# Optimization experiments

Measured on AMD Instinct MI355X. Metric: run time of the kernel, lower is better.

## Reference

```python
import jax, jax.numpy as jnp
import numpy as np

N_HEADS = 16
HEAD_DIM = 64
HIDDEN = N_HEADS * HEAD_DIM


def setup_inputs() -> dict:
    key = jax.random.key(0)
    ks = jax.random.split(key, 10)
    B, F, T = 2, 2048, 2048
    std = 0.02
    inp = {
        "from_tensor": jax.random.normal(ks[0], (B, F, HIDDEN), dtype=jnp.float32),
        "to_tensor": jax.random.normal(ks[1], (B, T, HIDDEN), dtype=jnp.float32),
        "attention_mask": jax.random.randint(ks[2], (B, F, T), 0, 2, dtype=jnp.int32),
        "Wq": jax.random.normal(ks[3], (HIDDEN, HIDDEN), dtype=jnp.float32) * std,
        "bq": jnp.zeros((HIDDEN,), dtype=jnp.float32),
        "Wk": jax.random.normal(ks[4], (HIDDEN, HIDDEN), dtype=jnp.float32) * std,
        "bk": jnp.zeros((HIDDEN,), dtype=jnp.float32),
        "Wv": jax.random.normal(ks[5], (HIDDEN, HIDDEN), dtype=jnp.float32) * std,
        "bv": jnp.zeros((HIDDEN,), dtype=jnp.float32),
    }
    return inp


def reference(from_tensor, to_tensor, attention_mask, Wq, bq, Wk, bk, Wv, bv):
    B, F, _ = from_tensor.shape
    T = to_tensor.shape[1]
    N, H = N_HEADS, HEAD_DIM

    # QKV projections (no activations: query/key/value act fns are None)
    q = (from_tensor @ Wq + bq).reshape(B, F, N, H)
    k = (to_tensor @ Wk + bk).reshape(B, T, N, H)
    v = (to_tensor @ Wv + bv).reshape(B, T, N, H)

    scores = jnp.einsum('BFNH,BTNH->BNFT', q, k) * (1.0 / np.sqrt(float(H)))
    # additive mask: mask [B,F,T] -> [B,1,F,T]; 0 entries get -10000
    adder = (1.0 - attention_mask.astype(jnp.float32))[:, None, :, :] * -10000.0
    scores = scores + adder
    probs = jax.nn.softmax(scores, axis=-1)  # dropout skipped (inference)

    context = jnp.einsum('BNFT,BTNH->BFNH', probs, v)
    return context.reshape(B, F, N * H)
```

## Files before the change

### kernel.cpp

```cpp
#include <hip/hip_runtime.h>


typedef short v8s __attribute__((ext_vector_type(8)));
typedef float v4f __attribute__((ext_vector_type(4)));
typedef unsigned short u16;
typedef unsigned int   u32;
typedef unsigned long long u64;

constexpr float QSCALE = 0.18033688011112042f;

__device__ __forceinline__ u16 f2bf(float f) {
    u32 u = __builtin_bit_cast(u32, f);
    u += 0x7fffu + ((u >> 16) & 1u);
    return (u16)(u >> 16);
}

__device__ __forceinline__ u32 pack_trunc(float a, float b) {
    return __builtin_amdgcn_perm(__builtin_bit_cast(u32, b),
                                 __builtin_bit_cast(u32, a), 0x07060302u);
}

__device__ __forceinline__ u32 pack_rnd(u32 ua, u32 ub) {
    ua += 0x7fffu + ((ua >> 16) & 1u);
    ub += 0x7fffu + ((ub >> 16) & 1u);
    return __builtin_amdgcn_perm(ub, ua, 0x07060302u);
}

__device__ __forceinline__ uint4 cvt8(uint4 lo, uint4 hi) {
    uint4 r;
    r.x = pack_rnd(lo.x, lo.y);
    r.y = pack_rnd(lo.z, lo.w);
    r.z = pack_rnd(hi.x, hi.y);
    r.w = pack_rnd(hi.z, hi.w);
    return r;
}

__device__ __forceinline__ v8s ld8(const u16* p) {
    return *reinterpret_cast<const v8s*>(p);
}

__global__ __launch_bounds__(256) void prep(
    const float* __restrict__ Wq, const float* __restrict__ Wk, const float* __restrict__ Wv,
    u16* __restrict__ Wqt, u16* __restrict__ Wkt, u16* __restrict__ Wvt,
    const int* __restrict__ mask, u64* __restrict__ words) {
    __shared__ float tile[32][33];
    const int bid = blockIdx.x, tid = threadIdx.x;
    if (bid < 3072) {
        const int zz = bid >> 10, rem = bid & 1023;
        const float* W = zz == 0 ? Wq : (zz == 1 ? Wk : Wv);
        u16* Wt = zz == 0 ? Wqt : (zz == 1 ? Wkt : Wvt);
        const int tx = tid & 31, ty = tid >> 5;
        const int n0 = (rem & 31) * 32, k0 = (rem >> 5) * 32;
        for (int i = 0; i < 4; i++)
            tile[ty + i * 8][tx] = W[(size_t)(k0 + ty + i * 8) * 1024 + n0 + tx];
        __syncthreads();
        for (int i = 0; i < 4; i++)
            Wt[(size_t)(n0 + ty + i * 8) * 1024 + k0 + tx] = f2bf(tile[tx][ty + i * 8]);
    } else {
        const int lane = tid & 63;
        const int g0 = (bid - 3072) * 32 + (tid >> 6) * 8;
        const int* mp = mask + (size_t)g0 * 64 + lane;
        u64* wp = words + g0;
        #pragma unroll
        for (int i = 0; i < 8; i++) {
            const u64 bits = __ballot(mp[(size_t)i * 64] != 0);
            if (lane == 0) wp[i] = bits;
        }
    }
}

__global__ __launch_bounds__(256, 3) void gemm_qkv(
    const float* __restrict__ Xf32, const float* __restrict__ Xt32,
    const u16* __restrict__ Wqt, const u16* __restrict__ Wkt, const u16* __restrict__ Wvt,
    const float* __restrict__ bq, const float* __restrict__ bk, const float* __restrict__ bv,
    u16* __restrict__ Qb, u16* __restrict__ Kb, u16* __restrict__ Vtb) {
    const int z = blockIdx.z;
    const float* A    = z == 0 ? Xf32 : Xt32;
    const u16* Bt     = z == 0 ? Wqt : (z == 1 ? Wkt : Wvt);
    const float* bias = z == 0 ? bq : (z == 1 ? bk : bv);
    u16* C            = z == 0 ? Qb : (z == 1 ? Kb : Vtb);
    const int mode    = (z == 2);
    const float sc    = (z == 0) ? QSCALE : 1.0f;

    __shared__ u16 As[2][128][32];
    __shared__ u16 Bs[2][128][32];
    const uint4* Ag = reinterpret_cast<const uint4*>(A);
    const uint4* Bg = reinterpret_cast<const uint4*>(Bt);

    const int tid = threadIdx.x;
    const int lane = tid & 63, wave = tid >> 6;
    const int quad = lane >> 4, l16 = lane & 15;
    const int wm = wave >> 1, wn = wave & 1;
    const int m0 = blockIdx.x * 128, n0 = blockIdx.y * 128;

    const int cg  = (lane & 3) ^ ((lane >> 3) & 3);
    const int sw8 = (quad ^ ((l16 >> 1) & 3)) * 8;

    const int gi0 = wave * 4;
    const uint4 *ap0, *ap1, *ap2, *ap3, *bp0, *bp1, *bp2, *bp3;
    {
        const int rl = lane >> 2;
        const int rb0 = ((gi0 + 0) & 7) * 16 + rl, kh0 = (gi0 + 0) >> 3;
        const int rb1 = ((gi0 + 1) & 7) * 16 + rl, kh1 = (gi0 + 1) >> 3;
        const int rb2 = ((gi0 + 2) & 7) * 16 + rl, kh2 = (gi0 + 2) >> 3;
        const int rb3 = ((gi0 + 3) & 7) * 16 + rl, kh3 = (gi0 + 3) >> 3;
        ap0 = Ag + (size_t)(m0 + rb0) * 256 + (kh0 * 4 + cg) * 2;
        ap1 = Ag + (size_t)(m0 + rb1) * 256 + (kh1 * 4 + cg) * 2;
        ap2 = Ag + (size_t)(m0 + rb2) * 256 + (kh2 * 4 + cg) * 2;
        ap3 = Ag + (size_t)(m0 + rb3) * 256 + (kh3 * 4 + cg) * 2;
        bp0 = Bg + (size_t)(n0 + rb0) * 128 + kh0 * 4 + cg;
        bp1 = Bg + (size_t)(n0 + rb1) * 128 + kh1 * 4 + cg;
        bp2 = Bg + (size_t)(n0 + rb2) * 128 + kh2 * 4 + cg;
        bp3 = Bg + (size_t)(n0 + rb3) * 128 + kh3 * 4 + cg;
    }
    uint4* da = reinterpret_cast<uint4*>((u16*)As + gi0 * 512) + lane;
    uint4* db = reinterpret_cast<uint4*>((u16*)Bs + gi0 * 512) + lane;

    v4f acc[4][4];
    for (int i = 0; i < 4; i++)
        for (int j = 0; j < 4; j++) acc[i][j] = (v4f)0.0f;

    uint4 a0l = ap0[0], a0h = ap0[1]; ap0 += 16;
    uint4 a1l = ap1[0], a1h = ap1[1]; ap1 += 16;
    uint4 a2l = ap2[0], a2h = ap2[1]; ap2 += 16;
    uint4 a3l = ap3[0], a3h = ap3[1]; ap3 += 16;
    uint4 sb0 = *bp0; bp0 += 8;
    uint4 sb1 = *bp1; bp1 += 8;
    uint4 sb2 = *bp2; bp2 += 8;
    uint4 sb3 = *bp3; bp3 += 8;
    uint4 ca0 = cvt8(a0l, a0h);
    uint4 ca1 = cvt8(a1l, a1h);
    uint4 ca2 = cvt8(a2l, a2h);
    uint4 ca3 = cvt8(a3l, a3h);

    for (int k0 = 0; k0 < 16; k0++) {
        __syncthreads();
        da[0]   = ca0;  da[64]  = ca1;  da[128] = ca2;  da[192] = ca3;
        db[0]   = sb0;  db[64]  = sb1;  db[128] = sb2;  db[192] = sb3;
        __syncthreads();

        if (k0 < 15) {
            a0l = ap0[0]; a0h = ap0[1]; ap0 += 16;
            a1l = ap1[0]; a1h = ap1[1]; ap1 += 16;
            a2l = ap2[0]; a2h = ap2[1]; ap2 += 16;
            a3l = ap3[0]; a3h = ap3[1]; ap3 += 16;
            sb0 = *bp0; bp0 += 8;
            sb1 = *bp1; bp1 += 8;
            sb2 = *bp2; bp2 += 8;
            sb3 = *bp3; bp3 += 8;
        }

        #pragma unroll
        for (int kk = 0; kk < 2; kk++) {
            v8s af[4], bf[4];
            #pragma unroll
            for (int mt = 0; mt < 4; mt++) af[mt] = ld8(&As[kk][wm * 64 + mt * 16 + l16][sw8]);
            #pragma unroll
            for (int nt = 0; nt < 4; nt++) bf[nt] = ld8(&Bs[kk][wn * 64 + nt * 16 + l16][sw8]);
            #pragma unroll
            for (int mt = 0; mt < 4; mt++)
                #pragma unroll
                for (int nt = 0; nt < 4; nt++)
                    acc[mt][nt] = __builtin_amdgcn_mfma_f32_16x16x32_bf16(af[mt], bf[nt], acc[mt][nt], 0, 0, 0);
        }

        if (k0 < 15) {
            ca0 = cvt8(a0l, a0h);
            ca1 = cvt8(a1l, a1h);
            ca2 = cvt8(a2l, a2h);
            ca3 = cvt8(a3l, a3h);
        }
    }

    #pragma unroll
    for (int nt = 0; nt < 4; nt++) {
        const int col = n0 + wn * 64 + nt * 16 + l16;
        const float bvv = bias[col];
        #pragma unroll
        for (int mt = 0; mt < 4; mt++) {
            const int mbase = m0 + wm * 64 + mt * 16 + quad * 4;
            if (mode == 0) {
                for (int r = 0; r < 4; r++)
                    C[(size_t)(mbase + r) * 1024 + col] = f2bf((acc[mt][nt][r] + bvv) * sc);
            } else {
                const int b = mbase >> 11, t = mbase & 2047;
                const int head = col >> 6, h = col & 63;
                ushort4 pk;
                pk.x = f2bf(acc[mt][nt][0] + bvv);
                pk.y = f2bf(acc[mt][nt][1] + bvv);
                pk.z = f2bf(acc[mt][nt][2] + bvv);
                pk.w = f2bf(acc[mt][nt][3] + bvv);
                *reinterpret_cast<ushort4*>(&C[(size_t)((b * 16 + head) * 64 + h) * 2048 + t]) = pk;
            }
        }
    }
}

__global__ __launch_bounds__(512, 4) void attn_fused(
    const u16* __restrict__ Qb, const u16* __restrict__ Kb,
    const u16* __restrict__ Vtb, const u64* __restrict__ mw,
    float* __restrict__ out) {
    __shared__ u16 Ks[2][2][64][32];
    __shared__ u16 Vs[2][2][64][32];
    __shared__ u32 Ps[8 * 1152];

    const int tid = threadIdx.x;
    const int lane = tid & 63, wave = tid >> 6;
    const int quad = lane >> 4, l16 = lane & 15;
    const int fwave = wave & 3, tw = wave >> 2;
    const int b = blockIdx.x >> 4, head = blockIdx.x & 15;
    const int f0 = blockIdx.y * 128;

    const uint4* Kg = reinterpret_cast<const uint4*>(Kb);
    const uint4* Vg = reinterpret_cast<const uint4*>(Vtb);
    const size_t vbase4 = (size_t)(b * 16 + head) * 64 * 256;

    const int cg  = (lane & 3) ^ ((lane >> 3) & 3);
    const int sw8 = (quad ^ ((l16 >> 1) & 3)) * 8;

    v8s qf[2][2];
    #pragma unroll
    for (int kk = 0; kk < 2; kk++)
        #pragma unroll
        for (int qh = 0; qh < 2; qh++)
            qf[kk][qh] = ld8(Qb + ((size_t)(b * 2048 + f0 + fwave * 32 + qh * 16 + l16) * 16 + head) * 64
                                + kk * 32 + quad * 8);

    v8s ones;
    #pragma unroll
    for (int i = 0; i < 8; i++) ones[i] = (short)0x3F80;

    const uint4 *sp0, *sp1, *sp2, *sp3;
    u16 *sd;
    size_t sinc;
    {
        const int rl = lane >> 2;
        if (wave < 4) {
            const int g0 = wave * 4;
            sd = (u16*)Ks + g0 * 512;
            sinc = 8192;
            #define KPTR(g) (Kg + ((size_t)(b * 2048 + ((g) >> 3) * 1024 + ((g) & 3) * 16 + rl) * 16 + head) * 8 \
                                + (((g) >> 2) & 1) * 4 + cg)
            sp0 = KPTR(g0); sp1 = KPTR(g0 + 1); sp2 = KPTR(g0 + 2); sp3 = KPTR(g0 + 3);
            #undef KPTR
        } else {
            const int g0 = (wave - 4) * 4;
            sd = (u16*)Vs + g0 * 512;
            sinc = 8;
            #define VPTR(g) (Vg + vbase4 + (size_t)(((g) & 3) * 16 + rl) * 256 + ((g) >> 3) * 128 \
                                + (((g) >> 2) & 1) * 4 + cg)
            sp0 = VPTR(g0); sp1 = VPTR(g0 + 1); sp2 = VPTR(g0 + 2); sp3 = VPTR(g0 + 3);
            #undef VPTR
        }
    }
    uint4* sd4 = reinterpret_cast<uint4*>(sd) + lane;

    v4f accO[2][4], accL[2];
    #pragma unroll
    for (int qh = 0; qh < 2; qh++) {
        accL[qh] = (v4f)0.0f;
        for (int ht = 0; ht < 4; ht++) accO[qh][ht] = (v4f)0.0f;
    }

    u32* myPs = Ps + wave * 1152;
    const u64* mrow = mw + (size_t)(b * 2048 + f0 + fwave * 32 + l16) * 32 + tw * 16;

    uint4 st0 = *sp0; sp0 += sinc;
    uint4 st1 = *sp1; sp1 += sinc;
    uint4 st2 = *sp2; sp2 += sinc;
    uint4 st3 = *sp3; sp3 += sinc;

    for (int it = 0; it < 16; it++) {
        __syncthreads();
        sd4[0]   = st0;
        sd4[64]  = st1;
        sd4[128] = st2;
        sd4[192] = st3;
        __syncthreads();

        if (it < 15) {
            st0 = *sp0; sp0 += sinc;
            st1 = *sp1; sp1 += sinc;
            st2 = *sp2; sp2 += sinc;
            st3 = *sp3; sp3 += sinc;
        }

        v4f s[2][4];
        #pragma unroll
        for (int qh = 0; qh < 2; qh++)
            for (int mt = 0; mt < 4; mt++) s[qh][mt] = (v4f)0.0f;
        #pragma unroll
        for (int kk = 0; kk < 2; kk++) {
            v8s kf[4];
            #pragma unroll
            for (int mt = 0; mt < 4; mt++) kf[mt] = ld8(&Ks[tw][kk][mt * 16 + l16][sw8]);
            #pragma unroll
            for (int qh = 0; qh < 2; qh++)
                #pragma unroll
                for (int mt = 0; mt < 4; mt++)
                    s[qh][mt] = __builtin_amdgcn_mfma_f32_16x16x32_bf16(kf[mt], qf[kk][qh], s[qh][mt], 0, 0, 0);
        }

        u32 pk[2][8];
        #pragma unroll
        for (int qh = 0; qh < 2; qh++) {
            const u64 w = mrow[qh * 512 + it];
            const u32 lo = (u32)(w >> (quad * 4));
            const u32 hi = (u32)(w >> (quad * 4 + 32));
            #pragma unroll
            for (int mt = 0; mt < 4; mt++) {
                const u32 bits = ((mt & 2) ? hi : lo) >> ((mt & 1) * 16);
                float p[4];
                #pragma unroll
                for (int r = 0; r < 4; r++) {
                    const float e = __builtin_amdgcn_exp2f(s[qh][mt][r]);
                    p[r] = ((bits >> r) & 1u) ? e : 0.0f;
                }
                pk[qh][mt * 2]     = pack_trunc(p[0], p[1]);
                pk[qh][mt * 2 + 1] = pack_trunc(p[2], p[3]);
            }
        }

        #pragma unroll
        for (int qh = 0; qh < 2; qh++) {
            const int row = qh * 16 + l16;
            #pragma unroll
            for (int mt = 0; mt < 4; mt++)
                *reinterpret_cast<uint2*>(&myPs[row * 36 + mt * 8 + quad * 2]) =
                    make_uint2(pk[qh][mt * 2], pk[qh][mt * 2 + 1]);
        }

        #pragma unroll
        for (int kk = 0; kk < 2; kk++) {
            v8s vf[4];
            #pragma unroll
            for (int ht = 0; ht < 4; ht++) vf[ht] = ld8(&Vs[tw][kk][ht * 16 + l16][sw8]);
            #pragma unroll
            for (int qh = 0; qh < 2; qh++) {
                const v8s pf = *reinterpret_cast<const v8s*>(
                    &myPs[(qh * 16 + l16) * 36 + kk * 16 + quad * 4]);
                #pragma unroll
                for (int ht = 0; ht < 4; ht++)
                    accO[qh][ht] = __builtin_amdgcn_mfma_f32_16x16x32_bf16(vf[ht], pf, accO[qh][ht], 0, 0, 0);
                accL[qh] = __builtin_amdgcn_mfma_f32_16x16x32_bf16(ones, pf, accL[qh], 0, 0, 0);
            }
        }
    }

    __syncthreads();
    float* fb = (float*)Ps;
    if (tw == 1) {
        float* wdst = fb + fwave * 2304 + lane * 36;
        #pragma unroll
        for (int qh = 0; qh < 2; qh++)
            #pragma unroll
            for (int ht = 0; ht < 4; ht++)
                *reinterpret_cast<v4f*>(wdst + (qh * 4 + ht) * 4) = accO[qh][ht];
        wdst[32] = accL[0][0];
        wdst[33] = accL[1][0];
    }
    __syncthreads();
    if (tw == 0) {
        const float* rsrc = fb + fwave * 2304 + lane * 36;
        float inv[2];
        #pragma unroll
        for (int qh = 0; qh < 2; qh++)
            inv[qh] = 1.0f / (accL[qh][0] + rsrc[32 + qh]);
        #pragma unroll
        for (int qh = 0; qh < 2; qh++) {
            const size_t ro = (size_t)(b * 2048 + f0 + fwave * 32 + qh * 16 + l16) * 1024 + head * 64;
            #pragma unroll
            for (int ht = 0; ht < 4; ht++) {
                const v4f p = *reinterpret_cast<const v4f*>(rsrc + (qh * 4 + ht) * 4);
                float4 o;
                o.x = (accO[qh][ht][0] + p[0]) * inv[qh];
                o.y = (accO[qh][ht][1] + p[1]) * inv[qh];
                o.z = (accO[qh][ht][2] + p[2]) * inv[qh];
                o.w = (accO[qh][ht][3] + p[3]) * inv[qh];
                *reinterpret_cast<float4*>(&out[ro + ht * 16 + quad * 4]) = o;
            }
        }
    }
}

extern "C" void kernel_launch(void* const* d_in, const int* in_sizes, int n_in,
                              void* d_out, int out_size, void* d_ws, size_t ws_size,
                              hipStream_t stream) {
    const float* from = (const float*)d_in[0];
    const float* to   = (const float*)d_in[1];
    const int*   mask = (const int*)d_in[2];
    const float* Wq = (const float*)d_in[3];
    const float* bq = (const float*)d_in[4];
    const float* Wk = (const float*)d_in[5];
    const float* bk = (const float*)d_in[6];
    const float* Wv = (const float*)d_in[7];
    const float* bv = (const float*)d_in[8];
    float* out = (float*)d_out;

    u16* Wqt = (u16*)d_ws;
    u16* Wkt = Wqt + 1048576;
    u16* Wvt = Wkt + 1048576;
    u16* Qb  = Wvt + 1048576;
    u16* Kb  = Qb  + 4194304;
    u16* Vtb = Kb  + 4194304;
    u64* mwords = (u64*)(Vtb + 4194304);

    prep<<<7168, 256, 0, stream>>>(Wq, Wk, Wv, Wqt, Wkt, Wvt, mask, mwords);

    gemm_qkv<<<dim3(32, 8, 3), 256, 0, stream>>>(from, to, Wqt, Wkt, Wvt, bq, bk, bv,
                                                 Qb, Kb, Vtb);

    attn_fused<<<dim3(32, 16), 512, 0, stream>>>(Qb, Kb, Vtb, mwords, out);
}
```

Measured before the change: 212.6 us.

## Double-buffer K in LDS and load V fragments directly from global

K tiles are now double-buffered in shared memory with all eight waves staging K, so each iteration needs one barrier instead of two. V is no longer staged through LDS. Each wave loads its V MFMA fragments straight from global memory early in the iteration, hoping the latency hides behind the QK MFMAs. This removes the LDS round-trip and a barrier. In exchange, the four f-waves fetch the same V data redundantly from global/L2, and load latency is exposed in the inner loop.

```diff
diff --git a/kernel.cpp b/kernel.cpp
--- a/kernel.cpp
+++ b/kernel.cpp
@@ -200,8 +200,7 @@
     const u16* __restrict__ Qb, const u16* __restrict__ Kb,
     const u16* __restrict__ Vtb, const u64* __restrict__ mw,
     float* __restrict__ out) {
-    __shared__ u16 Ks[2][2][64][32];
-    __shared__ u16 Vs[2][2][64][32];
+    __shared__ u16 Ks[2][2][2][64][32];
     __shared__ u32 Ps[8 * 1152];
 
     const int tid = threadIdx.x;
@@ -212,8 +211,7 @@
     const int f0 = blockIdx.y * 128;
 
     const uint4* Kg = reinterpret_cast<const uint4*>(Kb);
-    const uint4* Vg = reinterpret_cast<const uint4*>(Vtb);
-    const size_t vbase4 = (size_t)(b * 16 + head) * 64 * 256;
+    const size_t vb16 = (size_t)(b * 16 + head) * 131072;
 
     const int cg  = (lane & 3) ^ ((lane >> 3) & 3);
     const int sw8 = (quad ^ ((l16 >> 1) & 3)) * 8;
@@ -230,30 +228,17 @@
     #pragma unroll
     for (int i = 0; i < 8; i++) ones[i] = (short)0x3F80;
 
-    const uint4 *sp0, *sp1, *sp2, *sp3;
-    u16 *sd;
-    size_t sinc;
+    const uint4 *sp0, *sp1;
     {
         const int rl = lane >> 2;
-        if (wave < 4) {
-            const int g0 = wave * 4;
-            sd = (u16*)Ks + g0 * 512;
-            sinc = 8192;
-            #define KPTR(g) (Kg + ((size_t)(b * 2048 + ((g) >> 3) * 1024 + ((g) & 3) * 16 + rl) * 16 + head) * 8 \
-                                + (((g) >> 2) & 1) * 4 + cg)
-            sp0 = KPTR(g0); sp1 = KPTR(g0 + 1); sp2 = KPTR(g0 + 2); sp3 = KPTR(g0 + 3);
-            #undef KPTR
-        } else {
-            const int g0 = (wave - 4) * 4;
-            sd = (u16*)Vs + g0 * 512;
-            sinc = 8;
-            #define VPTR(g) (Vg + vbase4 + (size_t)(((g) & 3) * 16 + rl) * 256 + ((g) >> 3) * 128 \
-                                + (((g) >> 2) & 1) * 4 + cg)
-            sp0 = VPTR(g0); sp1 = VPTR(g0 + 1); sp2 = VPTR(g0 + 2); sp3 = VPTR(g0 + 3);
-            #undef VPTR
-        }
-    }
-    uint4* sd4 = reinterpret_cast<uint4*>(sd) + lane;
+        const int g0 = wave * 2;
+        #define KPTR(g) (Kg + ((size_t)(b * 2048 + ((g) >> 3) * 1024 + ((g) & 3) * 16 + rl) * 16 + head) * 8 \
+                            + (((g) >> 2) & 1) * 4 + cg)
+        sp0 = KPTR(g0); sp1 = KPTR(g0 + 1);
+        #undef KPTR
+    }
+    uint4* sd4a = reinterpret_cast<uint4*>((u16*)Ks + wave * 1024) + lane;
+    uint4* sd4b = reinterpret_cast<uint4*>((u16*)Ks + 8192 + wave * 1024) + lane;
 
     v4f accO[2][4], accL[2];
     #pragma unroll
@@ -265,25 +250,32 @@
     u32* myPs = Ps + wave * 1152;
     const u64* mrow = mw + (size_t)(b * 2048 + f0 + fwave * 32 + l16) * 32 + tw * 16;
 
-    uint4 st0 = *sp0; sp0 += sinc;
-    uint4 st1 = *sp1; sp1 += sinc;
-    uint4 st2 = *sp2; sp2 += sinc;
-    uint4 st3 = *sp3; sp3 += sinc;
+    uint4 k0a = *sp0; sp0 += 8192;
+    uint4 k0b = *sp1; sp1 += 8192;
+    sd4a[0]  = k0a;
+    sd4a[64] = k0b;
+    k0a = *sp0; sp0 += 8192;
+    k0b = *sp1; sp1 += 8192;
+    __syncthreads();
 
     for (int it = 0; it < 16; it++) {
-        __syncthreads();
-        sd4[0]   = st0;
-        sd4[64]  = st1;
-        sd4[128] = st2;
-        sd4[192] = st3;
-        __syncthreads();
-
         if (it < 15) {
-            st0 = *sp0; sp0 += sinc;
-            st1 = *sp1; sp1 += sinc;
-            st2 = *sp2; sp2 += sinc;
-            st3 = *sp3; sp3 += sinc;
-        }
+            uint4* wd = (it & 1) ? sd4a : sd4b;
+            wd[0]  = k0a;
+            wd[64] = k0b;
+            if (it < 14) {
+                k0a = *sp0; sp0 += 8192;
+                k0b = *sp1; sp1 += 8192;
+            }
+        }
+
+        const u16* vpi = Vtb + vb16 + tw * 1024 + it * 64 + quad * 8;
+        v8s vf0[4];
+        #pragma unroll
+        for (int ht = 0; ht < 4; ht++)
+            vf0[ht] = ld8(vpi + (size_t)(ht * 16 + l16) * 2048);
+
+        const u16* kb = (const u16*)Ks + (it & 1) * 8192;
 
         v4f s[2][4];
         #pragma unroll
@@ -293,7 +285,8 @@
         for (int kk = 0; kk < 2; kk++) {
             v8s kf[4];
             #pragma unroll
-            for (int mt = 0; mt < 4; mt++) kf[mt] = ld8(&Ks[tw][kk][mt * 16 + l16][sw8]);
+            for (int mt = 0; mt < 4; mt++)
+                kf[mt] = ld8(kb + tw * 4096 + kk * 2048 + (mt * 16 + l16) * 32 + sw8);
             #pragma unroll
             for (int qh = 0; qh < 2; qh++)
                 #pragma unroll
@@ -334,7 +327,9 @@
         for (int kk = 0; kk < 2; kk++) {
             v8s vf[4];
             #pragma unroll
-            for (int ht = 0; ht < 4; ht++) vf[ht] = ld8(&Vs[tw][kk][ht * 16 + l16][sw8]);
+            for (int ht = 0; ht < 4; ht++)
+                vf[ht] = (kk == 0) ? vf0[ht]
+                                   : ld8(vpi + (size_t)(ht * 16 + l16) * 2048 + 32);
             #pragma unroll
             for (int qh = 0; qh < 2; qh++) {
                 const v8s pf = *reinterpret_cast<const v8s*>(
@@ -345,9 +340,10 @@
                 accL[qh] = __builtin_amdgcn_mfma_f32_16x16x32_bf16(ones, pf, accL[qh], 0, 0, 0);
             }
         }
-    }
-
-    __syncthreads();
+
+        __syncthreads();
+    }
+
     float* fb = (float*)Ps;
     if (tw == 1) {
         float* wdst = fb + fwave * 2304 + lane * 36;
```

Result: slower. 273.1 us (+28.5%).
